# Kernel optimization log

Hardware: AMD Instinct MI355X
Metric: run time of the kernel (lower is better)

The kernel has to match this reference:

```python
import jax, jax.numpy as jnp
import numpy as np

N_NODES = 50000


def _gcn_conv(x, edge_index, W, b):
    # x: [N, F_in], edge_index: [2, E] (with self-loops already added)
    n = x.shape[0]
    src, dst = edge_index[0], edge_index[1]
    h = x @ W  # [N, F_out] transform first (as in PyG GCNConv)
    deg = jax.ops.segment_sum(jnp.ones_like(dst, dtype=h.dtype), dst, num_segments=n)
    dinv = jax.lax.rsqrt(jnp.maximum(deg, 1.0))  # self-loops guarantee deg >= 1
    norm = dinv[src] * dinv[dst]  # [E]
    msg = h[src] * norm[:, None]  # [E, F_out] gather + scale
    out = jax.ops.segment_sum(msg, dst, num_segments=n)  # scatter-add to targets
    return out + b


def setup_inputs() -> dict:
    key = jax.random.key(0)
    k1, k2, k3, k4 = jax.random.split(key, 4)
    num_features, hidden, num_classes = 128, 128, 16
    n, e = N_NODES, 800000
    x = jax.random.normal(k1, (n, num_features), dtype=jnp.float32)
    edge_index = jax.random.randint(k2, (2, e), 0, n, dtype=jnp.int64)
    # add self-loops (PyG GCNConv default add_self_loops=True)
    loops = jnp.arange(n, dtype=jnp.int64)
    edge_index = jnp.concatenate([edge_index, jnp.stack([loops, loops])], axis=1)
    s1 = 1.0 / np.sqrt(num_features)
    s2 = 1.0 / np.sqrt(hidden)
    W1 = jax.random.uniform(k3, (num_features, hidden), jnp.float32, -s1, s1)
    b1 = jnp.zeros((hidden,), jnp.float32)
    W2 = jax.random.uniform(k4, (hidden, num_classes), jnp.float32, -s2, s2)
    b2 = jnp.zeros((num_classes,), jnp.float32)
    return {"x": x, "edge_index": edge_index, "W1": W1, "b1": b1, "W2": W2, "b2": b2}


def reference(x, edge_index, W1, b1, W2, b2):
    h = jax.nn.relu(_gcn_conv(x, edge_index, W1, b1))
    # dropout is identity in eval mode (deterministic reference)
    h = _gcn_conv(h, edge_index, W2, b2)
    return jax.nn.log_softmax(h, axis=1)
```

## Files before the change

kernel.cpp:

```cpp
#include <hip/hip_runtime.h>


typedef unsigned int uint32;
typedef unsigned short u16;
typedef __attribute__((ext_vector_type(8))) short bf16x8;
typedef __attribute__((ext_vector_type(4))) float f32x4;

#define NBMAX 1024
#define CHUNK 4096
#define EH 8192

__device__ inline u16 bf16rn(float f) {
    unsigned u = __float_as_uint(f);
    return (u16)((u + 0x7fffu + ((u >> 16) & 1u)) >> 16);
}

__device__ inline void bffma(float2& a, float w, uint32 u) {
    a.x = fmaf(w, __uint_as_float(u << 16), a.x);
    a.y = fmaf(w, __uint_as_float(u & 0xffff0000u), a.y);
}

__global__ __launch_bounds__(256) void k_combo(
    const float* __restrict__ x, const float* __restrict__ W1,
    const int* __restrict__ dstv, int* __restrict__ partials,
    u16* __restrict__ h, int N, int E, int NB, int ntile)
{
    __shared__ __align__(16) unsigned char smem[128 * 136 * 2];
    int t = threadIdx.x;

    if ((int)blockIdx.x >= ntile) {
        int* hl = (int*)smem;
        int hb = blockIdx.x - ntile;
        int e0 = hb * EH, e1 = min(e0 + EH, E);
        for (int i = t; i < NB; i += 256) hl[i] = 0;
        __syncthreads();
        for (int e = e0 + t; e < e1; e += 256)
            atomicAdd(&hl[dstv[e] >> 8], 1);
        __syncthreads();
        int* pr = partials + (size_t)hb * NBMAX;
        for (int i = t; i < NB; i += 256) pr[i] = hl[i];
        return;
    }

    u16* Wl = (u16*)smem;
    const float4* Wg4 = (const float4*)W1;
    for (int g = t; g < 128 * 32; g += 256) {
        int k = g >> 5, n4 = (g & 31) * 4;
        float4 v = Wg4[g];
        Wl[(n4 + 0) * 136 + k] = bf16rn(v.x);
        Wl[(n4 + 1) * 136 + k] = bf16rn(v.y);
        Wl[(n4 + 2) * 136 + k] = bf16rn(v.z);
        Wl[(n4 + 3) * 136 + k] = bf16rn(v.w);
    }
    __syncthreads();

    int wave = t >> 6, lane = t & 63;
    int quad = lane >> 4, ln = lane & 15;
    int rowbase = blockIdx.x * 64 + wave * 16;
    int rclamp = min(rowbase + ln, N - 1);

    f32x4 acc[8];
    #pragma unroll
    for (int ct = 0; ct < 8; ++ct) acc[ct] = (f32x4){0.f, 0.f, 0.f, 0.f};

    #pragma unroll
    for (int q = 0; q < 4; ++q) {
        const float4* xr = (const float4*)(x + (size_t)rclamp * 128 + q * 32 + quad * 8);
        float4 a0 = xr[0], a1 = xr[1];
        bf16x8 afr;
        afr[0] = (short)bf16rn(a0.x); afr[1] = (short)bf16rn(a0.y);
        afr[2] = (short)bf16rn(a0.z); afr[3] = (short)bf16rn(a0.w);
        afr[4] = (short)bf16rn(a1.x); afr[5] = (short)bf16rn(a1.y);
        afr[6] = (short)bf16rn(a1.z); afr[7] = (short)bf16rn(a1.w);
        #pragma unroll
        for (int ct = 0; ct < 8; ++ct) {
            bf16x8 bfr = *(const bf16x8*)&Wl[(ct * 16 + ln) * 136 + q * 32 + quad * 8];
            acc[ct] = __builtin_amdgcn_mfma_f32_16x16x32_bf16(afr, bfr, acc[ct], 0, 0, 0);
        }
    }
    #pragma unroll
    for (int i = 0; i < 4; ++i) {
        int r = rowbase + quad * 4 + i;
        if (r < N) {
            u16* hp = h + (size_t)r * 128 + ln;
            #pragma unroll
            for (int ct = 0; ct < 8; ++ct)
                hp[ct * 16] = bf16rn(acc[ct][i]);
        }
    }
}

__global__ __launch_bounds__(1024) void k_scanB(
    const int* __restrict__ partials, int* __restrict__ bbase,
    int* __restrict__ bfill, int NB, int E, int NH)
{
    __shared__ int s[1024];
    int t = threadIdx.x;
    int v = 0;
    if (t < NB)
        for (int p = 0; p < NH; ++p) v += partials[(size_t)p * NBMAX + t];
    s[t] = v;
    __syncthreads();
    for (int off = 1; off < 1024; off <<= 1) {
        int u = (t >= off) ? s[t - off] : 0;
        __syncthreads();
        s[t] += u;
        __syncthreads();
    }
    if (t < NB) {
        bbase[t] = s[t] - v;
        bfill[t] = 0;
    }
    if (t == 0) bbase[NB] = E;
}

__global__ __launch_bounds__(256) void k_partition(
    const int* __restrict__ src, const int* __restrict__ dstv,
    const int* __restrict__ bbase, int* __restrict__ bfill,
    uint32* __restrict__ tmp, int E, int NB)
{
    __shared__ int cntL[NBMAX];
    __shared__ int baseL[NBMAX];
    int t = threadIdx.x;
    int e0 = blockIdx.x * CHUNK;
    int e1 = min(e0 + CHUNK, E);
    for (int i = t; i < NB; i += 256) cntL[i] = 0;
    __syncthreads();
    for (int e = e0 + t; e < e1; e += 256)
        atomicAdd(&cntL[dstv[e] >> 8], 1);
    __syncthreads();
    for (int i = t; i < NB; i += 256) {
        int cc = cntL[i];
        baseL[i] = cc ? bbase[i] + atomicAdd(&bfill[i], cc) : 0;
        cntL[i] = 0;
    }
    __syncthreads();
    for (int e = e0 + t; e < e1; e += 256) {
        int sv = src[e], d = dstv[e];
        int b = d >> 8;
        int r = atomicAdd(&cntL[b], 1);
        tmp[baseL[b] + r] = (uint32)sv | ((uint32)(d & 255) << 16);
    }
}

__global__ __launch_bounds__(256) void k_bsort(
    const uint32* __restrict__ tmp, const int* __restrict__ bbase,
    u16* __restrict__ ssrc, int* __restrict__ rs,
    float* __restrict__ dinv, int N)
{
    __shared__ int cnt[256];
    __shared__ int ofs[256];
    int t = threadIdx.x;
    int b = blockIdx.x;
    int base = bbase[b];
    int endb = bbase[b + 1];
    int node0 = b << 8;

    cnt[t] = 0;
    __syncthreads();
    for (int i = base + t; i < endb; i += 256)
        atomicAdd(&cnt[(tmp[i] >> 16) & 255], 1);
    __syncthreads();
    int v = cnt[t];
    __syncthreads();
    for (int off = 1; off < 256; off <<= 1) {
        int u = (t >= off) ? cnt[t - off] : 0;
        __syncthreads();
        cnt[t] += u;
        __syncthreads();
    }
    int node = node0 + t;
    if (node < N) {
        dinv[node] = rsqrtf(fmaxf((float)v, 1.0f));
        rs[node] = base + cnt[t];
    }
    ofs[t] = base + cnt[t] - v;
    __syncthreads();
    for (int i = base + t; i < endb; i += 256) {
        uint32 rec = tmp[i];
        int pos = atomicAdd(&ofs[(rec >> 16) & 255], 1);
        ssrc[pos] = (u16)(rec & 0xffffu);
    }
}

__global__ __launch_bounds__(256) void k_pullg(
    const int* __restrict__ rs, const u16* __restrict__ ssrc,
    const float* __restrict__ dinv, const uint2* __restrict__ h,
    const float* __restrict__ b1, const float* __restrict__ W2,
    u16* __restrict__ h2, int N)
{
    __shared__ float W2T[16 * 132];
    __shared__ float rowbuf[8 * 132];
    int t = threadIdx.x;

    for (int g = t; g < 2048; g += 256) {
        int k = g >> 4, f = g & 15;
        W2T[f * 132 + k] = W2[g];
    }

    int wave = t >> 6, lane = t & 63;
    int sub = lane >> 5;
    int rl = lane & 31;
    int rowbase = blockIdx.x * 8;
    int n = rowbase + wave * 2 + sub;
    bool valid = (n < N);
    int nc = valid ? n : 0;
    int start = valid ? ((nc == 0) ? 0 : rs[nc - 1]) : 0;
    int len   = valid ? (rs[nc] - start) : 0;
    float dn  = valid ? dinv[nc] : 0.f;
    int lenMax = max(len, __shfl_xor(len, 32));

    float2 aA[4], aB[4];
    #pragma unroll
    for (int k = 0; k < 4; ++k) {
        aA[k] = (float2){0.f, 0.f};
        aB[k] = (float2){0.f, 0.f};
    }

    for (int tt = 0; tt < lenMax; tt += 4) {
        int s[4];
        uint2 u[4];
        float w[4];
        #pragma unroll
        for (int k = 0; k < 4; ++k) {
            bool act = (tt + k) < len;
            int jj = act ? (start + tt + k) : 0;
            s[k] = (int)ssrc[jj];
            w[k] = act ? 1.f : 0.f;
        }
        #pragma unroll
        for (int k = 0; k < 4; ++k)
            u[k] = h[(size_t)s[k] * 32 + rl];
        #pragma unroll
        for (int k = 0; k < 4; ++k)
            w[k] *= dn * dinv[s[k]];
        #pragma unroll
        for (int k = 0; k < 4; ++k) {
            bffma(aA[k], w[k], u[k].x);
            bffma(aB[k], w[k], u[k].y);
        }
    }

    {
        int r = wave * 2 + sub;
        float4 bb = ((const float4*)b1)[rl];
        float4 v;
        v.x = fmaxf(((aA[0].x + aA[1].x) + (aA[2].x + aA[3].x)) + bb.x, 0.f);
        v.y = fmaxf(((aA[0].y + aA[1].y) + (aA[2].y + aA[3].y)) + bb.y, 0.f);
        v.z = fmaxf(((aB[0].x + aB[1].x) + (aB[2].x + aB[3].x)) + bb.z, 0.f);
        v.w = fmaxf(((aB[0].y + aB[1].y) + (aB[2].y + aB[3].y)) + bb.w, 0.f);
        ((float4*)rowbuf)[r * 33 + rl] = v;
    }
    __syncthreads();

    if (t < 128) {
        int f = t & 15, r = t >> 4;
        const float4* W4 = (const float4*)W2T;
        const float4* rb4 = (const float4*)rowbuf;
        float acc = 0.f;
        #pragma unroll 8
        for (int k4 = 0; k4 < 32; ++k4) {
            float4 w = W4[f * 33 + k4];
            float4 xv = rb4[r * 33 + k4];
            acc = fmaf(xv.x, w.x, acc);
            acc = fmaf(xv.y, w.y, acc);
            acc = fmaf(xv.z, w.z, acc);
            acc = fmaf(xv.w, w.w, acc);
        }
        int rn = rowbase + r;
        if (rn < N) h2[(size_t)rn * 16 + f] = bf16rn(acc);
    }
}

__global__ __launch_bounds__(256) void k_pull2(
    const int* __restrict__ rs, const u16* __restrict__ ssrc,
    const float* __restrict__ dinv, const uint32* __restrict__ h2,
    const float* __restrict__ b2, float* __restrict__ out, int N)
{
    int idx = blockIdx.x * 256 + threadIdx.x;
    int n = idx >> 3;
    if (n >= N) return;
    int c = idx & 7;
    int start = (n == 0) ? 0 : rs[n - 1];
    int len = rs[n] - start;
    float dn = dinv[n];

    float2 a[4];
    #pragma unroll
    for (int k = 0; k < 4; ++k) a[k] = (float2){0.f, 0.f};

    for (int tt = 0; tt < len; tt += 4) {
        int s[4];
        uint32 u[4];
        float w[4];
        #pragma unroll
        for (int k = 0; k < 4; ++k) {
            bool act = (tt + k) < len;
            int jj = act ? (start + tt + k) : 0;
            s[k] = (int)ssrc[jj];
            w[k] = act ? 1.f : 0.f;
        }
        #pragma unroll
        for (int k = 0; k < 4; ++k)
            u[k] = h2[(size_t)s[k] * 8 + c];
        #pragma unroll
        for (int k = 0; k < 4; ++k)
            w[k] *= dn * dinv[s[k]];
        #pragma unroll
        for (int k = 0; k < 4; ++k)
            bffma(a[k], w[k], u[k]);
    }

    float acc0 = (a[0].x + a[1].x) + (a[2].x + a[3].x);
    float acc1 = (a[0].y + a[1].y) + (a[2].y + a[3].y);
    float v0 = acc0 + b2[2 * c];
    float v1 = acc1 + b2[2 * c + 1];
    float m = fmaxf(v0, v1);
    #pragma unroll
    for (int off = 1; off < 8; off <<= 1) m = fmaxf(m, __shfl_xor(m, off));
    float s = expf(v0 - m) + expf(v1 - m);
    #pragma unroll
    for (int off = 1; off < 8; off <<= 1) s += __shfl_xor(s, off);
    float ls = logf(s);
    float2 r = {v0 - m - ls, v1 - m - ls};
    ((float2*)out)[(size_t)n * 8 + c] = r;
}

extern "C" void kernel_launch(void* const* d_in, const int* in_sizes, int n_in,
                              void* d_out, int out_size, void* d_ws, size_t ws_size,
                              hipStream_t stream) {
    const float* x  = (const float*)d_in[0];
    const int*   ei = (const int*)d_in[1];
    const float* W1 = (const float*)d_in[2];
    const float* b1 = (const float*)d_in[3];
    const float* W2 = (const float*)d_in[4];
    const float* b2 = (const float*)d_in[5];
    float* outp = (float*)d_out;

    const int E = in_sizes[1] / 2;
    const int N = in_sizes[0] / 128;
    const int NB = (N + 255) >> 8;
    const int NH = (E + EH - 1) / EH;
    const int ntile = (N + 63) / 64;
    const int* src  = ei;
    const int* dstv = ei + E;

    const int Npad = (N + 255) & ~255;
    const int Epad = (E + 255) & ~255;
    int*   partials = (int*)d_ws;
    int*   bbase = partials + 128 * NBMAX;
    int*   bfill = bbase + NBMAX + 256;
    int*   rs    = bfill + NBMAX;
    float* dinv  = (float*)(rs + Npad);
    uint32* tmp  = (uint32*)(dinv + Npad);
    u16*   ssrc  = (u16*)(tmp + Epad);
    u16*   h     = (u16*)(ssrc + Epad);
    u16*   h2    = h;

    k_combo<<<ntile + NH, 256, 0, stream>>>(x, W1, dstv, partials, h, N, E, NB, ntile);
    k_scanB<<<1, 1024, 0, stream>>>(partials, bbase, bfill, NB, E, NH);
    k_partition<<<(E + CHUNK - 1) / CHUNK, 256, 0, stream>>>(src, dstv, bbase,
                                                             bfill, tmp, E, NB);
    k_bsort<<<NB, 256, 0, stream>>>(tmp, bbase, ssrc, rs, dinv, N);
    k_pullg<<<(N + 7) / 8, 256, 0, stream>>>(rs, ssrc, dinv, (const uint2*)h,
                                             b1, W2, h2, N);
    k_pull2<<<(N * 8 + 255) / 256, 256, 0, stream>>>(rs, ssrc, dinv,
                                                     (const uint32*)h2, b2, outp, N);
}
```

Baseline: 190.8 us.

## Split layer-1 aggregation into feature-quarter blocks and separate the second GEMM

```diff
diff --git a/kernel.cpp b/kernel.cpp
--- a/kernel.cpp
+++ b/kernel.cpp
@@ -183,43 +183,36 @@
     }
 }
 
-__global__ __launch_bounds__(256) void k_pullg(
+__global__ __launch_bounds__(256) void k_pullq(
     const int* __restrict__ rs, const u16* __restrict__ ssrc,
-    const float* __restrict__ dinv, const uint2* __restrict__ h,
-    const float* __restrict__ b1, const float* __restrict__ W2,
-    u16* __restrict__ h2, int N)
-{
-    __shared__ float W2T[16 * 132];
-    __shared__ float rowbuf[8 * 132];
-    int t = threadIdx.x;
-
-    for (int g = t; g < 2048; g += 256) {
-        int k = g >> 4, f = g & 15;
-        W2T[f * 132 + k] = W2[g];
-    }
-
+    const float* __restrict__ dinv, const uint32* __restrict__ h32,
+    const float* __restrict__ b1, uint32* __restrict__ h1,
+    int N, int NG)
+{
+    int b = blockIdx.x;
+    int q = (b & 7) >> 1;
+    int g = (b >> 3) * 2 + (b & 1);
+    if (g >= NG) return;
+    int t = threadIdx.x;
     int wave = t >> 6, lane = t & 63;
-    int sub = lane >> 5;
-    int rl = lane & 31;
-    int rowbase = blockIdx.x * 8;
-    int n = rowbase + wave * 2 + sub;
+    int rr = lane >> 4;
+    int rl = lane & 15;
+    int n = g * 16 + wave * 4 + rr;
     bool valid = (n < N);
     int nc = valid ? n : 0;
     int start = valid ? ((nc == 0) ? 0 : rs[nc - 1]) : 0;
     int len   = valid ? (rs[nc] - start) : 0;
     float dn  = valid ? dinv[nc] : 0.f;
-    int lenMax = max(len, __shfl_xor(len, 32));
-
-    float2 aA[4], aB[4];
-    #pragma unroll
-    for (int k = 0; k < 4; ++k) {
-        aA[k] = (float2){0.f, 0.f};
-        aB[k] = (float2){0.f, 0.f};
-    }
-
-    for (int tt = 0; tt < lenMax; tt += 4) {
+    int m = max(len, __shfl_xor(len, 16));
+    m = max(m, __shfl_xor(m, 32));
+
+    float2 a[4];
+    #pragma unroll
+    for (int k = 0; k < 4; ++k) a[k] = (float2){0.f, 0.f};
+
+    for (int tt = 0; tt < m; tt += 4) {
         int s[4];
-        uint2 u[4];
+        uint32 u[4];
         float w[4];
         #pragma unroll
         for (int k = 0; k < 4; ++k) {
@@ -230,46 +223,63 @@
         }
         #pragma unroll
         for (int k = 0; k < 4; ++k)
-            u[k] = h[(size_t)s[k] * 32 + rl];
+            u[k] = h32[(size_t)s[k] * 64 + q * 16 + rl];
         #pragma unroll
         for (int k = 0; k < 4; ++k)
             w[k] *= dn * dinv[s[k]];
         #pragma unroll
-        for (int k = 0; k < 4; ++k) {
-            bffma(aA[k], w[k], u[k].x);
-            bffma(aB[k], w[k], u[k].y);
-        }
-    }
-
-    {
-        int r = wave * 2 + sub;
-        float4 bb = ((const float4*)b1)[rl];
-        float4 v;
-        v.x = fmaxf(((aA[0].x + aA[1].x) + (aA[2].x + aA[3].x)) + bb.x, 0.f);
-        v.y = fmaxf(((aA[0].y + aA[1].y) + (aA[2].y + aA[3].y)) + bb.y, 0.f);
-        v.z = fmaxf(((aB[0].x + aB[1].x) + (aB[2].x + aB[3].x)) + bb.z, 0.f);
-        v.w = fmaxf(((aB[0].y + aB[1].y) + (aB[2].y + aB[3].y)) + bb.w, 0.f);
-        ((float4*)rowbuf)[r * 33 + rl] = v;
-    }
-    __syncthreads();
-
-    if (t < 128) {
-        int f = t & 15, r = t >> 4;
-        const float4* W4 = (const float4*)W2T;
-        const float4* rb4 = (const float4*)rowbuf;
-        float acc = 0.f;
-        #pragma unroll 8
-        for (int k4 = 0; k4 < 32; ++k4) {
-            float4 w = W4[f * 33 + k4];
-            float4 xv = rb4[r * 33 + k4];
-            acc = fmaf(xv.x, w.x, acc);
-            acc = fmaf(xv.y, w.y, acc);
-            acc = fmaf(xv.z, w.z, acc);
-            acc = fmaf(xv.w, w.w, acc);
-        }
-        int rn = rowbase + r;
-        if (rn < N) h2[(size_t)rn * 16 + f] = bf16rn(acc);
-    }
+        for (int k = 0; k < 4; ++k)
+            bffma(a[k], w[k], u[k]);
+    }
+
+    if (valid) {
+        float2 bb = ((const float2*)b1)[q * 16 + rl];
+        float vx = fmaxf(((a[0].x + a[1].x) + (a[2].x + a[3].x)) + bb.x, 0.f);
+        float vy = fmaxf(((a[0].y + a[1].y) + (a[2].y + a[3].y)) + bb.y, 0.f);
+        h1[(size_t)n * 64 + q * 16 + rl] =
+            (uint32)bf16rn(vx) | ((uint32)bf16rn(vy) << 16);
+    }
+}
+
+__global__ __launch_bounds__(256) void k_gemm2(
+    const uint32* __restrict__ h1, const float* __restrict__ W2,
+    u16* __restrict__ h2, int N)
+{
+    __shared__ float W2T[16 * 132];
+    __shared__ float rb[16 * 132];
+    int t = threadIdx.x;
+    int n0 = blockIdx.x * 16;
+
+    for (int g = t; g < 2048; g += 256) {
+        int k = g >> 4, f = g & 15;
+        W2T[f * 132 + k] = W2[g];
+    }
+    for (int g = t; g < 1024; g += 256) {
+        int row = g >> 6, j = g & 63;
+        int n = min(n0 + row, N - 1);
+        uint32 v = h1[(size_t)n * 64 + j];
+        float2 d;
+        d.x = __uint_as_float(v << 16);
+        d.y = __uint_as_float(v & 0xffff0000u);
+        *(float2*)&rb[row * 132 + 2 * j] = d;
+    }
+    __syncthreads();
+
+    int f = t & 15, r = t >> 4;
+    const float4* W4 = (const float4*)W2T;
+    const float4* rb4 = (const float4*)rb;
+    float acc = 0.f;
+    #pragma unroll 8
+    for (int k4 = 0; k4 < 32; ++k4) {
+        float4 w = W4[f * 33 + k4];
+        float4 xv = rb4[r * 33 + k4];
+        acc = fmaf(xv.x, w.x, acc);
+        acc = fmaf(xv.y, w.y, acc);
+        acc = fmaf(xv.z, w.z, acc);
+        acc = fmaf(xv.w, w.w, acc);
+    }
+    int rn = n0 + r;
+    if (rn < N) h2[(size_t)rn * 16 + f] = bf16rn(acc);
 }
 
 __global__ __launch_bounds__(256) void k_pull2(
@@ -342,6 +352,7 @@
     const int NB = (N + 255) >> 8;
     const int NH = (E + EH - 1) / EH;
     const int ntile = (N + 63) / 64;
+    const int NG = (N + 15) / 16;
     const int* src  = ei;
     const int* dstv = ei + E;
 
@@ -354,16 +365,20 @@
     float* dinv  = (float*)(rs + Npad);
     uint32* tmp  = (uint32*)(dinv + Npad);
     u16*   ssrc  = (u16*)(tmp + Epad);
-    u16*   h     = (u16*)(ssrc + Epad);
-    u16*   h2    = h;
+    uintptr_t hp = ((uintptr_t)(ssrc + Epad) + 255) & ~(uintptr_t)255;
+    u16*   h     = (u16*)hp;
+    u16*   h1    = h + (size_t)Npad * 128;
+    u16*   h2    = h1 + (size_t)Npad * 128;
 
     k_combo<<<ntile + NH, 256, 0, stream>>>(x, W1, dstv, partials, h, N, E, NB, ntile);
     k_scanB<<<1, 1024, 0, stream>>>(partials, bbase, bfill, NB, E, NH);
     k_partition<<<(E + CHUNK - 1) / CHUNK, 256, 0, stream>>>(src, dstv, bbase,
                                                              bfill, tmp, E, NB);
     k_bsort<<<NB, 256, 0, stream>>>(tmp, bbase, ssrc, rs, dinv, N);
-    k_pullg<<<(N + 7) / 8, 256, 0, stream>>>(rs, ssrc, dinv, (const uint2*)h,
-                                             b1, W2, h2, N);
+    k_pullq<<<8 * ((NG + 1) / 2), 256, 0, stream>>>(rs, ssrc, dinv,
+                                                    (const uint32*)h, b1,
+                                                    (uint32*)h1, N, NG);
+    k_gemm2<<<NG, 256, 0, stream>>>((const uint32*)h1, W2, h2, N);
     k_pull2<<<(N * 8 + 255) / 256, 256, 0, stream>>>(rs, ssrc, dinv,
                                                      (const uint32*)h2, b2, outp, N);
 }
```

Result: slower. 214.9 us (+12.7%).

## Replace two-level bucket sort CSR build with global-atomic degree count and scatter

Applied to the files above, without the earlier changes.

```diff
diff --git a/kernel.cpp b/kernel.cpp
--- a/kernel.cpp
+++ b/kernel.cpp
@@ -6,8 +6,6 @@
 typedef __attribute__((ext_vector_type(8))) short bf16x8;
 typedef __attribute__((ext_vector_type(4))) float f32x4;
 
-#define NBMAX 1024
-#define CHUNK 4096
 #define EH 8192
 
 __device__ inline u16 bf16rn(float f) {
@@ -22,23 +20,17 @@
 
 __global__ __launch_bounds__(256) void k_combo(
     const float* __restrict__ x, const float* __restrict__ W1,
-    const int* __restrict__ dstv, int* __restrict__ partials,
-    u16* __restrict__ h, int N, int E, int NB, int ntile)
+    const int* __restrict__ dstv, int* __restrict__ deg,
+    u16* __restrict__ h, int N, int E, int ntile)
 {
     __shared__ __align__(16) unsigned char smem[128 * 136 * 2];
     int t = threadIdx.x;
 
     if ((int)blockIdx.x >= ntile) {
-        int* hl = (int*)smem;
         int hb = blockIdx.x - ntile;
         int e0 = hb * EH, e1 = min(e0 + EH, E);
-        for (int i = t; i < NB; i += 256) hl[i] = 0;
-        __syncthreads();
         for (int e = e0 + t; e < e1; e += 256)
-            atomicAdd(&hl[dstv[e] >> 8], 1);
-        __syncthreads();
-        int* pr = partials + (size_t)hb * NBMAX;
-        for (int i = t; i < NB; i += 256) pr[i] = hl[i];
+            atomicAdd(&deg[dstv[e]], 1);
         return;
     }
 
@@ -90,97 +82,69 @@
     }
 }
 
-__global__ __launch_bounds__(1024) void k_scanB(
-    const int* __restrict__ partials, int* __restrict__ bbase,
-    int* __restrict__ bfill, int NB, int E, int NH)
-{
-    __shared__ int s[1024];
+__global__ __launch_bounds__(256) void k_scan1(
+    const int* __restrict__ deg, int* __restrict__ rs,
+    float* __restrict__ dinv, int* __restrict__ bsum, int N)
+{
+    __shared__ int s[256];
     int t = threadIdx.x;
-    int v = 0;
-    if (t < NB)
-        for (int p = 0; p < NH; ++p) v += partials[(size_t)p * NBMAX + t];
-    s[t] = v;
+    int n = blockIdx.x * 256 + t;
+    int d = (n < N) ? deg[n] : 0;
+    s[t] = d;
     __syncthreads();
-    for (int off = 1; off < 1024; off <<= 1) {
+    for (int off = 1; off < 256; off <<= 1) {
         int u = (t >= off) ? s[t - off] : 0;
         __syncthreads();
         s[t] += u;
         __syncthreads();
     }
-    if (t < NB) {
-        bbase[t] = s[t] - v;
-        bfill[t] = 0;
-    }
-    if (t == 0) bbase[NB] = E;
-}
-
-__global__ __launch_bounds__(256) void k_partition(
-    const int* __restrict__ src, const int* __restrict__ dstv,
-    const int* __restrict__ bbase, int* __restrict__ bfill,
-    uint32* __restrict__ tmp, int E, int NB)
-{
-    __shared__ int cntL[NBMAX];
-    __shared__ int baseL[NBMAX];
+    if (n < N) {
+        rs[n] = s[t];
+        dinv[n] = rsqrtf(fmaxf((float)d, 1.0f));
+    }
+    if (t == 255) bsum[blockIdx.x] = s[255];
+}
+
+__global__ __launch_bounds__(256) void k_scan2(
+    const int* __restrict__ bsum, int* __restrict__ bofs, int NBg)
+{
+    __shared__ int s[256];
     int t = threadIdx.x;
-    int e0 = blockIdx.x * CHUNK;
-    int e1 = min(e0 + CHUNK, E);
-    for (int i = t; i < NB; i += 256) cntL[i] = 0;
-    __syncthreads();
-    for (int e = e0 + t; e < e1; e += 256)
-        atomicAdd(&cntL[dstv[e] >> 8], 1);
-    __syncthreads();
-    for (int i = t; i < NB; i += 256) {
-        int cc = cntL[i];
-        baseL[i] = cc ? bbase[i] + atomicAdd(&bfill[i], cc) : 0;
-        cntL[i] = 0;
-    }
-    __syncthreads();
-    for (int e = e0 + t; e < e1; e += 256) {
-        int sv = src[e], d = dstv[e];
-        int b = d >> 8;
-        int r = atomicAdd(&cntL[b], 1);
-        tmp[baseL[b] + r] = (uint32)sv | ((uint32)(d & 255) << 16);
-    }
-}
-
-__global__ __launch_bounds__(256) void k_bsort(
-    const uint32* __restrict__ tmp, const int* __restrict__ bbase,
-    u16* __restrict__ ssrc, int* __restrict__ rs,
-    float* __restrict__ dinv, int N)
-{
-    __shared__ int cnt[256];
-    __shared__ int ofs[256];
-    int t = threadIdx.x;
-    int b = blockIdx.x;
-    int base = bbase[b];
-    int endb = bbase[b + 1];
-    int node0 = b << 8;
-
-    cnt[t] = 0;
-    __syncthreads();
-    for (int i = base + t; i < endb; i += 256)
-        atomicAdd(&cnt[(tmp[i] >> 16) & 255], 1);
-    __syncthreads();
-    int v = cnt[t];
+    int v = (t < NBg) ? bsum[t] : 0;
+    s[t] = v;
     __syncthreads();
     for (int off = 1; off < 256; off <<= 1) {
-        int u = (t >= off) ? cnt[t - off] : 0;
+        int u = (t >= off) ? s[t - off] : 0;
         __syncthreads();
-        cnt[t] += u;
+        s[t] += u;
         __syncthreads();
     }
-    int node = node0 + t;
-    if (node < N) {
-        dinv[node] = rsqrtf(fmaxf((float)v, 1.0f));
-        rs[node] = base + cnt[t];
-    }
-    ofs[t] = base + cnt[t] - v;
-    __syncthreads();
-    for (int i = base + t; i < endb; i += 256) {
-        uint32 rec = tmp[i];
-        int pos = atomicAdd(&ofs[(rec >> 16) & 255], 1);
-        ssrc[pos] = (u16)(rec & 0xffffu);
-    }
+    bofs[t] = s[t] - v;
+}
+
+__global__ __launch_bounds__(256) void k_scan3(
+    int* __restrict__ rs, const int* __restrict__ deg,
+    const int* __restrict__ bofs, int* __restrict__ sta,
+    int* __restrict__ fill, int N)
+{
+    int n = blockIdx.x * 256 + threadIdx.x;
+    if (n >= N) return;
+    int r = rs[n] + bofs[n >> 8];
+    rs[n] = r;
+    sta[n] = r - deg[n];
+    fill[n] = 0;
+}
+
+__global__ __launch_bounds__(256) void k_scatter(
+    const int* __restrict__ src, const int* __restrict__ dstv,
+    const int* __restrict__ sta, int* __restrict__ fill,
+    u16* __restrict__ ssrc, int E)
+{
+    int e = blockIdx.x * 256 + threadIdx.x;
+    if (e >= E) return;
+    int s = src[e], d = dstv[e];
+    int pos = sta[d] + atomicAdd(&fill[d], 1);
+    ssrc[pos] = (u16)s;
 }
 
 __global__ __launch_bounds__(256) void k_pullg(
@@ -347,21 +311,24 @@
 
     const int Npad = (N + 255) & ~255;
     const int Epad = (E + 255) & ~255;
-    int*   partials = (int*)d_ws;
-    int*   bbase = partials + 128 * NBMAX;
-    int*   bfill = bbase + NBMAX + 256;
-    int*   rs    = bfill + NBMAX;
-    float* dinv  = (float*)(rs + Npad);
-    uint32* tmp  = (uint32*)(dinv + Npad);
-    u16*   ssrc  = (u16*)(tmp + Epad);
-    u16*   h     = (u16*)(ssrc + Epad);
-    u16*   h2    = h;
-
-    k_combo<<<ntile + NH, 256, 0, stream>>>(x, W1, dstv, partials, h, N, E, NB, ntile);
-    k_scanB<<<1, 1024, 0, stream>>>(partials, bbase, bfill, NB, E, NH);
-    k_partition<<<(E + CHUNK - 1) / CHUNK, 256, 0, stream>>>(src, dstv, bbase,
-                                                             bfill, tmp, E, NB);
-    k_bsort<<<NB, 256, 0, stream>>>(tmp, bbase, ssrc, rs, dinv, N);
+    int*   deg  = (int*)d_ws;
+    int*   rs   = deg + Npad;
+    int*   sta  = rs + Npad;
+    int*   fill = sta + Npad;
+    int*   bsum = fill + Npad;
+    int*   bofs = bsum + 256;
+    float* dinv = (float*)(bofs + 256);
+    u16*   ssrc = (u16*)(dinv + Npad);
+    uintptr_t hp = ((uintptr_t)(ssrc + Epad) + 255) & ~(uintptr_t)255;
+    u16*   h    = (u16*)hp;
+    u16*   h2   = h + (size_t)Npad * 128;
+
+    hipMemsetAsync(deg, 0, (size_t)Npad * sizeof(int), stream);
+    k_combo<<<ntile + NH, 256, 0, stream>>>(x, W1, dstv, deg, h, N, E, ntile);
+    k_scan1<<<NB, 256, 0, stream>>>(deg, rs, dinv, bsum, N);
+    k_scan2<<<1, 256, 0, stream>>>(bsum, bofs, NB);
+    k_scan3<<<NB, 256, 0, stream>>>(rs, deg, bofs, sta, fill, N);
+    k_scatter<<<(E + 255) / 256, 256, 0, stream>>>(src, dstv, sta, fill, ssrc, E);
     k_pullg<<<(N + 7) / 8, 256, 0, stream>>>(rs, ssrc, dinv, (const uint2*)h,
                                              b1, W2, h2, N);
     k_pull2<<<(N * 8 + 255) / 256, 256, 0, stream>>>(rs, ssrc, dinv,
```

After: 213.6 us. +12.0%, slower.
